# Kernel optimization log

Measured on AMD Instinct MI355X. Metric: run time of the kernel, lower is better.

Reference implementation:

```python
import jax, jax.numpy as jnp
from jax import lax
import numpy as np

B, S, T = 32, 512, 64
IN, H, L, HC, OUT = 512, 512, 2, 4, 512

def setup_inputs() -> dict:
    key = jax.random.key(0)
    ks = jax.random.split(key, 12)
    def w(k, shape, fan_in):
        return (jax.random.normal(k, shape, jnp.float32) / np.float32(np.sqrt(fan_in)))
    lstm_in0 = IN + HC * H
    return {
        "inputs": jax.random.normal(ks[0], (B, T, IN), jnp.float32),
        "lengths": jax.random.randint(ks[1], (B,), 1, S + 1),
        "final_hiddens": jax.random.normal(ks[2], (L, B, H), jnp.float32),
        "hiddens": jax.random.normal(ks[3], (B, S, H), jnp.float32),
        "max_output_len": T,
        "max_seq_len": S,
        "Wa1": w(ks[4], (H, 2 * H), 2 * H), "ba1": jnp.zeros((H,), jnp.float32),
        "Wa2": w(ks[5], (HC, H), H), "ba2": jnp.zeros((HC,), jnp.float32),
        "W_ih0": w(ks[6], (4 * H, lstm_in0), lstm_in0), "W_hh0": w(ks[7], (4 * H, H), H),
        "b_ih0": jnp.zeros((4 * H,), jnp.float32), "b_hh0": jnp.zeros((4 * H,), jnp.float32),
        "W_ih1": w(ks[8], (4 * H, H), H), "W_hh1": w(ks[9], (4 * H, H), H),
        "b_ih1": jnp.zeros((4 * H,), jnp.float32), "b_hh1": jnp.zeros((4 * H,), jnp.float32),
        "Wo1": w(ks[10], (H, (1 + HC) * H), (1 + HC) * H), "bo1": jnp.zeros((H,), jnp.float32),
        "Wo2": w(ks[11], (OUT, H), H), "bo2": jnp.zeros((OUT,), jnp.float32),
    }

def _lstm_cell(x, h, c, W_ih, W_hh, b_ih, b_hh):
    # PyTorch LSTM gate order: i, f, g, o
    g = x @ W_ih.T + b_ih + h @ W_hh.T + b_hh
    i, f, gg, o = jnp.split(g, 4, axis=-1)
    c_new = jax.nn.sigmoid(f) * c + jax.nn.sigmoid(i) * jnp.tanh(gg)
    h_new = jax.nn.sigmoid(o) * jnp.tanh(c_new)
    return h_new, c_new

def reference(inputs, lengths, final_hiddens, hiddens, max_output_len, max_seq_len,
              Wa1, ba1, Wa2, ba2, W_ih0, W_hh0, b_ih0, b_hh0,
              W_ih1, W_hh1, b_ih1, b_hh1, Wo1, bo1, Wo2, bo2):
    batch = inputs.shape[0]
    # r_mask[b, s] = 1 if s < lengths[b] else 0  -> [B, S, 1]
    r_mask = (jnp.arange(max_seq_len)[None, :] < lengths[:, None]).astype(hiddens.dtype)[..., None]

    def step(carry, x_t):
        h, c = carry  # each [L, B, H]
        last = h[-1]  # [B, H]
        dup = last[:, None, :] * r_mask  # [B, S, H]
        a = jax.nn.relu(jnp.concatenate([dup, hiddens], axis=2) @ Wa1.T + ba1)  # [B,S,H]
        a = jax.nn.relu(a @ Wa2.T + ba2)  # [B,S,HC]
        a = jax.nn.softmax(a, axis=1)  # softmax over seq dim (unmasked, as in source)
        c_vecs = jnp.einsum('bsk,bsh->bkh', a, hiddens).reshape(batch, -1)  # [B, HC*H]
        x = jnp.concatenate([x_t, c_vecs], axis=1)  # [B, IN + HC*H]
        h0, c0 = _lstm_cell(x, h[0], c[0], W_ih0, W_hh0, b_ih0, b_hh0)
        h1, c1 = _lstm_cell(h0, h[1], c[1], W_ih1, W_hh1, b_ih1, b_hh1)
        out = jnp.tanh(jax.nn.relu(jnp.concatenate([h1, c_vecs], axis=1) @ Wo1.T + bo1) @ Wo2.T + bo2)
        return (jnp.stack([h0, h1]), jnp.stack([c0, c1])), out

    c_init = jnp.zeros_like(final_hiddens)
    _, outs = lax.scan(step, (final_hiddens, c_init), jnp.swapaxes(inputs, 0, 1))  # [T,B,OUT]
    return jnp.swapaxes(outs, 0, 1)  # [B, T, OUT]
```

## Files before the change

### kernel.cpp

```cpp
#include <hip/hip_runtime.h>
#include <cmath>


typedef unsigned short ushort;
typedef unsigned int uint;
typedef __attribute__((ext_vector_type(8))) short bf16x8;
typedef __attribute__((ext_vector_type(4))) float f32x4;

__device__ __forceinline__ float sigmoidf_(float x) { return 1.f / (1.f + __expf(-x)); }
__device__ __forceinline__ float bf2f(ushort u) {
  union { uint i; float f; } x; x.i = ((uint)u) << 16; return x.f;
}
__device__ __forceinline__ ushort f2bf(float f) {
  union { float f; uint i; } x; x.f = f;
  return (ushort)((x.i + 0x7FFFu + ((x.i >> 16) & 1u)) >> 16);
}
__device__ __forceinline__ float wave_sum(float v) {
#pragma unroll
  for (int m = 1; m < 64; m <<= 1) v += __shfl_xor(v, m, 64);
  return v;
}
__device__ __forceinline__ float wave_max(float v) {
#pragma unroll
  for (int m = 1; m < 64; m <<= 1) v = fmaxf(v, __shfl_xor(v, m, 64));
  return v;
}

__global__ void __launch_bounds__(256) k_init(const float* __restrict__ fh,
                                              ushort* h0b0, ushort* h1b0,
                                              float* c0, float* c1) {
  int i = blockIdx.x * 256 + threadIdx.x;
  h0b0[i] = f2bf(fh[i]);
  h1b0[i] = f2bf(fh[16384 + i]);
  c0[i] = 0.f; c1[i] = 0.f;
}

__global__ void __launch_bounds__(256) k_prep(const float* __restrict__ hid,
                                              ushort* __restrict__ hbf) {
  size_t i0 = ((size_t)blockIdx.x * 256 + threadIdx.x) * 8;
  float4 f0 = *(const float4*)&hid[i0];
  float4 f1 = *(const float4*)&hid[i0 + 4];
  uint4 o;
  o.x = (uint)f2bf(f0.x) | ((uint)f2bf(f0.y) << 16);
  o.y = (uint)f2bf(f0.z) | ((uint)f2bf(f0.w) << 16);
  o.z = (uint)f2bf(f1.x) | ((uint)f2bf(f1.y) << 16);
  o.w = (uint)f2bf(f1.z) | ((uint)f2bf(f1.w) << 16);
  *(uint4*)&hbf[i0] = o;
}

__global__ void __launch_bounds__(256) k_inprep(const float* __restrict__ inputs,
                                                ushort* __restrict__ inb) {
  size_t idx4 = ((size_t)blockIdx.x * 256 + threadIdx.x) * 4;
  int m = (int)(idx4 >> 9), k = (int)(idx4 & 511);
  int b = m & 31, tt = m >> 5;
  float4 v = *(const float4*)&inputs[((size_t)b * 64 + tt) * 512 + k];
  ushort4 o; o.x = f2bf(v.x); o.y = f2bf(v.y); o.z = f2bf(v.z); o.w = f2bf(v.w);
  *(ushort4*)&inb[(size_t)m * 512 + k] = o;
}

__global__ void __launch_bounds__(256) k_wcvt(const float* __restrict__ W1, int ld1,
                                              const float* __restrict__ W2, int ld2,
                                              int split, int K,
                                              ushort* __restrict__ dst) {
  size_t idx = ((size_t)blockIdx.x * 256 + threadIdx.x) * 4;
  int j = (int)(idx / K), k = (int)(idx % K);
  const float* src = (k < split) ? (W1 + (size_t)j * ld1 + k)
                                 : (W2 + (size_t)j * ld2 + (k - split));
  float4 v = *(const float4*)src;
  ushort4 o; o.x = f2bf(v.x); o.y = f2bf(v.y); o.z = f2bf(v.z); o.w = f2bf(v.w);
  *(ushort4*)&dst[idx] = o;
}

__global__ void __launch_bounds__(256) k_hidproj(const float* __restrict__ hid,
                                                 const float* __restrict__ Wa1,
                                                 ushort* __restrict__ hpb) {
  __shared__ float As[64][33];
  __shared__ float Bs[64][33];
  int tid = threadIdx.x;
  int r0 = blockIdx.x * 64;
  int n0 = blockIdx.y * 64;
  int tm = (tid >> 4) << 2, tn = (tid & 15) << 2;
  int lr = tid >> 2, lk = (tid & 3) << 3;
  float acc[4][4] = {};
  for (int k0 = 0; k0 < 512; k0 += 32) {
    float4 a0 = *(const float4*)&hid[(size_t)(r0 + lr) * 512 + k0 + lk];
    float4 a1 = *(const float4*)&hid[(size_t)(r0 + lr) * 512 + k0 + lk + 4];
    float4 b0 = *(const float4*)&Wa1[(size_t)(n0 + lr) * 1024 + 512 + k0 + lk];
    float4 b1 = *(const float4*)&Wa1[(size_t)(n0 + lr) * 1024 + 512 + k0 + lk + 4];
    __syncthreads();
    As[lr][lk+0]=a0.x; As[lr][lk+1]=a0.y; As[lr][lk+2]=a0.z; As[lr][lk+3]=a0.w;
    As[lr][lk+4]=a1.x; As[lr][lk+5]=a1.y; As[lr][lk+6]=a1.z; As[lr][lk+7]=a1.w;
    Bs[lr][lk+0]=b0.x; Bs[lr][lk+1]=b0.y; Bs[lr][lk+2]=b0.z; Bs[lr][lk+3]=b0.w;
    Bs[lr][lk+4]=b1.x; Bs[lr][lk+5]=b1.y; Bs[lr][lk+6]=b1.z; Bs[lr][lk+7]=b1.w;
    __syncthreads();
#pragma unroll 8
    for (int kk = 0; kk < 32; kk++) {
      float av[4], bv[4];
#pragma unroll
      for (int i = 0; i < 4; i++) av[i] = As[tm + i][kk];
#pragma unroll
      for (int j = 0; j < 4; j++) bv[j] = Bs[tn + j][kk];
#pragma unroll
      for (int i = 0; i < 4; i++)
#pragma unroll
        for (int j = 0; j < 4; j++) acc[i][j] += av[i] * bv[j];
    }
  }
#pragma unroll
  for (int i = 0; i < 4; i++) {
    ushort4 o;
    o.x = f2bf(acc[i][0]); o.y = f2bf(acc[i][1]);
    o.z = f2bf(acc[i][2]); o.w = f2bf(acc[i][3]);
    *(ushort4*)&hpb[(size_t)(r0 + tm + i) * 512 + n0 + tn] = o;
  }
}

__device__ __forceinline__ void scores_accum(const ushort* __restrict__ hpr,
                                             const float* __restrict__ wa2s,
                                             const float* __restrict__ ba1s,
                                             const float* __restrict__ qs, float m,
                                             float& a0, float& a1, float& a2,
                                             float& a3) {
#pragma unroll
  for (int i8 = 0; i8 < 8; i8++) {
    bf16x8 hv8 = *(const bf16x8*)(hpr + i8 * 8);
#pragma unroll
    for (int e = 0; e < 8; e++) {
      int i = i8 * 8 + e;
      float a = fmaxf(bf2f(((ushort*)&hv8)[e]) + ba1s[i] + m * qs[i], 0.f);
      a0 += wa2s[i] * a;
      a1 += wa2s[64 + i] * a;
      a2 += wa2s[128 + i] * a;
      a3 += wa2s[192 + i] * a;
    }
  }
}

__global__ void __launch_bounds__(512) k_scst(const ushort* __restrict__ hpb,
                                              const float* __restrict__ ba1,
                                              const float* __restrict__ Wa2,
                                              float4* __restrict__ scoresP4) {
  __shared__ float wa2s[256], ba1s[64], qz[64];
  int bid = blockIdx.x, tid = threadIdx.x;
  int b = bid >> 3, kdq = bid & 7, kd0 = kdq << 6, s = tid;
  if (tid < 256) wa2s[tid] = Wa2[(tid >> 6) * 512 + kd0 + (tid & 63)];
  else if (tid < 320) ba1s[tid - 256] = ba1[kd0 + (tid - 256)];
  else if (tid < 384) qz[tid - 320] = 0.f;
  __syncthreads();
  float a0 = 0.f, a1 = 0.f, a2 = 0.f, a3 = 0.f;
  const ushort* hpr = hpb + (size_t)(b * 512 + s) * 512 + kd0;
  scores_accum(hpr, wa2s, ba1s, qz, 0.f, a0, a1, a2, a3);
  scoresP4[((size_t)(kdq * 32 + b)) * 512 + s] = make_float4(a0, a1, a2, a3);
}

__global__ void __launch_bounds__(512) k_sum0(const float4* __restrict__ scoresP4,
                                              const float* __restrict__ ba2,
                                              float* __restrict__ scores0) {
  int idx = blockIdx.x * 512 + threadIdx.x;
  int b = idx >> 9, s = idx & 511;
  float a0 = ba2[0], a1 = ba2[1], a2 = ba2[2], a3 = ba2[3];
#pragma unroll
  for (int q = 0; q < 8; q++) {
    float4 p = scoresP4[((size_t)(q * 32 + b)) * 512 + s];
    a0 += p.x; a1 += p.y; a2 += p.z; a3 += p.w;
  }
  scores0[((size_t)b * 4 + 0) * 512 + s] = fmaxf(a0, 0.f);
  scores0[((size_t)b * 4 + 1) * 512 + s] = fmaxf(a1, 0.f);
  scores0[((size_t)b * 4 + 2) * 512 + s] = fmaxf(a2, 0.f);
  scores0[((size_t)b * 4 + 3) * 512 + s] = fmaxf(a3, 0.f);
}

__global__ void __launch_bounds__(512) k_stat0(const float* __restrict__ scores0,
                                               const int* __restrict__ lengths,
                                               float* __restrict__ m0v,
                                               float* __restrict__ statZ,
                                               float* __restrict__ P0) {
  __shared__ float st[32], st2[32];
  int b = blockIdx.x, tid = threadIdx.x, lane = tid & 63, w = tid >> 6;
  int s = tid, len = lengths[b];
  bool stat = s >= len;
  float v[4], m0[4];
#pragma unroll
  for (int k = 0; k < 4; k++) v[k] = scores0[((size_t)b * 4 + k) * 512 + s];
#pragma unroll
  for (int k = 0; k < 4; k++) {
    float mk = wave_max(stat ? v[k] : -1e30f);
    if (lane == 0) st[w * 4 + k] = mk;
  }
  __syncthreads();
#pragma unroll
  for (int k = 0; k < 4; k++) {
    float m = st[k];
#pragma unroll
    for (int w2 = 1; w2 < 8; w2++) m = fmaxf(m, st[w2 * 4 + k]);
    m0[k] = m;
  }
  float e[4];
#pragma unroll
  for (int k = 0; k < 4; k++) {
    e[k] = stat ? __expf(v[k] - m0[k]) : 0.f;
    float sk = wave_sum(e[k]);
    if (lane == 0) st2[w * 4 + k] = sk;
  }
  __syncthreads();
#pragma unroll
  for (int k = 0; k < 4; k++) {
    P0[((size_t)b * 4 + k) * 512 + s] = e[k];
  }
  if (tid == 0) {
#pragma unroll
    for (int k = 0; k < 4; k++) {
      float z = 0.f;
#pragma unroll
      for (int w2 = 0; w2 < 8; w2++) z += st2[w2 * 4 + k];
      m0v[b * 4 + k] = m0[k];
      statZ[b * 4 + k] = z;
    }
  }
}

__global__ void __launch_bounds__(512) k_statvec(const float* __restrict__ P0,
                                                 const ushort* __restrict__ hbf,
                                                 const int* __restrict__ lengths,
                                                 float* __restrict__ statvec) {
  __shared__ float P[4 * 512];
  __shared__ float red2[8 * 256];
  int bid = blockIdx.x, tid = threadIdx.x;
  int b = bid >> 3, hs = bid & 7;
#pragma unroll
  for (int k = 0; k < 4; k++) P[k * 512 + tid] = P0[((size_t)b * 4 + k) * 512 + tid];
  __syncthreads();
  int h = tid & 63, w8 = tid >> 6;
  int len = lengths[b];
  float a0 = 0.f, a1 = 0.f, a2 = 0.f, a3 = 0.f;
  for (int si = len + ((w8 - len) & 7); si < 512; si += 8) {
    float hv = bf2f(hbf[((size_t)(b * 512 + si) * 512) + (hs << 6) + h]);
    a0 += P[si] * hv;
    a1 += P[512 + si] * hv;
    a2 += P[1024 + si] * hv;
    a3 += P[1536 + si] * hv;
  }
  red2[(w8 << 8) + h] = a0;
  red2[(w8 << 8) + 64 + h] = a1;
  red2[(w8 << 8) + 128 + h] = a2;
  red2[(w8 << 8) + 192 + h] = a3;
  __syncthreads();
  if (tid < 256) {
    int k = tid >> 6, hh = tid & 63;
    float acc = 0.f;
#pragma unroll
    for (int c = 0; c < 8; c++) acc += red2[(c << 8) + (k << 6) + hh];
    statvec[((size_t)b * 4 + k) * 512 + (hs << 6) + hh] = acc;
  }
}

__device__ __forceinline__ void mfma_slice(
    const ushort* __restrict__ W, int ldW, int jrow0, int jstride,
    const ushort* __restrict__ xA, int ldA, int xsplit,
    const ushort* __restrict__ xB, int ldB, int coff,
    int klo, int khi, float* __restrict__ redrow) {
  const int l = threadIdx.x & 63;
  const int r16 = l & 15, koff = (l >> 4) * 8;
  const int j = jrow0 + (r16 & 3) + (r16 >> 2) * jstride;
  const ushort* wrow = W + (size_t)j * ldW + koff;
  const ushort* a0A = xA + (size_t)r16 * ldA + koff;
  const ushort* a1A = xA + (size_t)(16 + r16) * ldA + koff;
  const ushort* a0B = xB + (size_t)r16 * ldB + koff;
  const ushort* a1B = xB + (size_t)(16 + r16) * ldB + koff;
  f32x4 acc0 = {0.f, 0.f, 0.f, 0.f}, acc1 = {0.f, 0.f, 0.f, 0.f};
#pragma unroll 4
  for (int k0 = klo; k0 < khi; k0 += 32) {
    bf16x8 av0, av1;
    if (k0 < xsplit) {
      av0 = *(const bf16x8*)(a0A + k0);
      av1 = *(const bf16x8*)(a1A + k0);
    } else {
      av0 = *(const bf16x8*)(a0B + (k0 - coff));
      av1 = *(const bf16x8*)(a1B + (k0 - coff));
    }
    bf16x8 wv = *(const bf16x8*)(wrow + k0);
    acc0 = __builtin_amdgcn_mfma_f32_16x16x32_bf16(av0, wv, acc0, 0, 0, 0);
    acc1 = __builtin_amdgcn_mfma_f32_16x16x32_bf16(av1, wv, acc1, 0, 0, 0);
  }
  const int brow = (l >> 4) << 2;
#pragma unroll
  for (int r = 0; r < 4; r++) {
    redrow[r16 * 33 + brow + r] = acc0[r];
    redrow[r16 * 33 + 16 + brow + r] = acc1[r];
  }
}

__global__ void __launch_bounds__(256) k_gin0(const ushort* __restrict__ Wg0b,
                                              const ushort* __restrict__ inb,
                                              float* __restrict__ gi0) {
  __shared__ float red[4 * 528];
  int tid = threadIdx.x, w = tid >> 6;
  int j0 = blockIdx.x * 16;
  for (int mt = 0; mt < 4; mt++) {
    int m0 = (blockIdx.y * 4 + mt) * 32;
    mfma_slice(Wg0b, 3072, j0, 4, inb + (size_t)m0 * 512, 512, 1 << 30,
               inb + (size_t)m0 * 512, 512, 0, w * 128, w * 128 + 128,
               red + w * 528);
    __syncthreads();
#pragma unroll
    for (int e = 0; e < 2; e++) {
      int idx = tid + e * 256;
      int j = idx >> 5, b = idx & 31;
      float v = 0.f;
#pragma unroll
      for (int ww = 0; ww < 4; ww++) v += red[ww * 528 + j * 33 + b];
      gi0[(size_t)(m0 + b) * 2048 + j0 + j] = v;
    }
    __syncthreads();
  }
}

__global__ void __launch_bounds__(512) k_scq(
    const ushort* __restrict__ Wq, const ushort* __restrict__ Wo1,
    const ushort* __restrict__ h1cur, const ushort* __restrict__ xb,
    const float* __restrict__ bo1, ushort* __restrict__ o1bf,
    const ushort* __restrict__ hpb, const float* __restrict__ ba1,
    const float* __restrict__ Wa2, const int* __restrict__ lengths,
    float4* __restrict__ scoresP4, int t) {
  __shared__ float red[8 * 528];
  __shared__ float qs[64], wa2s[256], ba1s[64];
  int bid = blockIdx.x, tid = threadIdx.x, w = tid >> 6, lane = tid & 63;
  if (bid < 32) {
    if (t < 1) return;
    mfma_slice(Wo1, 2560, bid * 16, 4, h1cur, 512, 512, xb, 2048, 512,
               w * 320, w * 320 + 320, red + w * 528);
    __syncthreads();
    int j = tid & 15, b = tid >> 4;
    float v = 0.f;
#pragma unroll
    for (int ww = 0; ww < 8; ww++) v += red[ww * 528 + j * 33 + b];
    int jj = bid * 16 + j;
    o1bf[b * 512 + jj] = f2bf(fmaxf(v + bo1[jj], 0.f));
  } else {
    if (t >= 64) return;
    int r = bid - 32;
    int b = r >> 3, kdq = r & 7, kd0 = kdq << 6;
    if (tid < 256) wa2s[tid] = Wa2[(tid >> 6) * 512 + kd0 + (tid & 63)];
    else if (tid < 320) ba1s[tid - 256] = ba1[kd0 + (tid - 256)];
    {
      bf16x8 hv8 = *(const bf16x8*)(h1cur + b * 512 + lane * 8);
      float hf[8];
#pragma unroll
      for (int e2 = 0; e2 < 8; e2++) hf[e2] = bf2f(((ushort*)&hv8)[e2]);
#pragma unroll
      for (int rr = 0; rr < 8; rr++) {
        int row = kd0 + w * 8 + rr;
        bf16x8 wv8 = *(const bf16x8*)(Wq + (size_t)row * 512 + lane * 8);
        float acc = 0.f;
#pragma unroll
        for (int e2 = 0; e2 < 8; e2++) acc += hf[e2] * bf2f(((ushort*)&wv8)[e2]);
        acc = wave_sum(acc);
        if (lane == 0) qs[w * 8 + rr] = acc;
      }
    }
    __syncthreads();
    int s = tid, len = lengths[b];
    if ((tid & ~63) >= len) return;
    float m = (s < len) ? 1.f : 0.f;
    float a0 = 0.f, a1 = 0.f, a2 = 0.f, a3 = 0.f;
    const ushort* hpr = hpb + (size_t)(b * 512 + s) * 512 + kd0;
    scores_accum(hpr, wa2s, ba1s, qs, m, a0, a1, a2, a3);
    scoresP4[((size_t)(kdq * 32 + b)) * 512 + s] = make_float4(a0, a1, a2, a3);
  }
}

__global__ void __launch_bounds__(512) k_ctxout(
    const float4* __restrict__ scoresP4, const float* __restrict__ ba2,
    const int* __restrict__ lengths, const ushort* __restrict__ hbf,
    const float* __restrict__ m0v, const float* __restrict__ statZ,
    const float* __restrict__ statvec, ushort* __restrict__ xb,
    const ushort* __restrict__ Wo2, const ushort* __restrict__ o1bf,
    const float* __restrict__ bo2, float* __restrict__ outp, int t) {
  __shared__ float red[8 * 528];
  __shared__ float P[4 * 512];
  __shared__ float red2[8 * 256];
  __shared__ float st[32], st2[32];
  int bid = blockIdx.x, tid = threadIdx.x;
  if (bid < 32) {
    if (t < 1) return;
    int w = tid >> 6;
    mfma_slice(Wo2, 512, bid * 16, 4, o1bf, 512, 1 << 30, o1bf, 512, 0,
               w * 64, w * 64 + 64, red + w * 528);
    __syncthreads();
    int j = tid & 15, b = tid >> 4;
    float v = 0.f;
#pragma unroll
    for (int ww = 0; ww < 8; ww++) v += red[ww * 528 + j * 33 + b];
    int jj = bid * 16 + j;
    outp[((size_t)b * 64 + (t - 1)) * 512 + jj] = tanhf(v + bo2[jj]);
  } else {
    if (t >= 64) return;
    int r = bid - 32;
    int b = r >> 3, hs = r & 7;
    int lane = tid & 63, w = tid >> 6;
    int s = tid, len = lengths[b];
    bool act = s < len;
    float v[4];
    {
      float a0 = ba2[0], a1 = ba2[1], a2 = ba2[2], a3 = ba2[3];
      if (act) {
#pragma unroll
        for (int q = 0; q < 8; q++) {
          float4 p = scoresP4[((size_t)(q * 32 + b)) * 512 + s];
          a0 += p.x; a1 += p.y; a2 += p.z; a3 += p.w;
        }
        v[0] = fmaxf(a0, 0.f); v[1] = fmaxf(a1, 0.f);
        v[2] = fmaxf(a2, 0.f); v[3] = fmaxf(a3, 0.f);
      } else {
        v[0] = v[1] = v[2] = v[3] = -1e30f;
      }
    }
    float M[4];
#pragma unroll
    for (int k = 0; k < 4; k++) {
      float mk = wave_max(v[k]);
      if (lane == 0) st[w * 4 + k] = mk;
    }
    __syncthreads();
#pragma unroll
    for (int k = 0; k < 4; k++) {
      float m = st[k];
#pragma unroll
      for (int w2 = 1; w2 < 8; w2++) m = fmaxf(m, st[w2 * 4 + k]);
      M[k] = fmaxf(m, m0v[b * 4 + k]);
    }
    float e[4];
#pragma unroll
    for (int k = 0; k < 4; k++) {
      e[k] = act ? __expf(v[k] - M[k]) : 0.f;
      float sk = wave_sum(e[k]);
      if (lane == 0) st2[w * 4 + k] = sk;
    }
    __syncthreads();
    float sc[4];
#pragma unroll
    for (int k = 0; k < 4; k++) {
      float dynZ = 0.f;
#pragma unroll
      for (int w2 = 0; w2 < 8; w2++) dynZ += st2[w2 * 4 + k];
      float scB = __expf(m0v[b * 4 + k] - M[k]);
      float Z = dynZ + scB * statZ[b * 4 + k];
      float invZ = 1.f / Z;
      P[k * 512 + s] = e[k] * invZ;
      sc[k] = scB * invZ;
    }
    __syncthreads();
    int h = tid & 63, w8 = tid >> 6;
    float a0 = 0.f, a1 = 0.f, a2 = 0.f, a3 = 0.f;
    const ushort* hb0 = hbf + ((size_t)b * 512) * 512 + (hs << 6) + h;
    int si = w8;
    for (; si + 24 < len; si += 32) {
      float h0v = bf2f(hb0[(size_t)si * 512]);
      float h1v = bf2f(hb0[(size_t)(si + 8) * 512]);
      float h2v = bf2f(hb0[(size_t)(si + 16) * 512]);
      float h3v = bf2f(hb0[(size_t)(si + 24) * 512]);
      a0 += P[si] * h0v + P[si + 8] * h1v + P[si + 16] * h2v + P[si + 24] * h3v;
      a1 += P[512 + si] * h0v + P[512 + si + 8] * h1v + P[512 + si + 16] * h2v +
            P[512 + si + 24] * h3v;
      a2 += P[1024 + si] * h0v + P[1024 + si + 8] * h1v + P[1024 + si + 16] * h2v +
            P[1024 + si + 24] * h3v;
      a3 += P[1536 + si] * h0v + P[1536 + si + 8] * h1v + P[1536 + si + 16] * h2v +
            P[1536 + si + 24] * h3v;
    }
    for (; si < len; si += 8) {
      float hv = bf2f(hb0[(size_t)si * 512]);
      a0 += P[si] * hv;
      a1 += P[512 + si] * hv;
      a2 += P[1024 + si] * hv;
      a3 += P[1536 + si] * hv;
    }
    red2[(w8 << 8) + h] = a0;
    red2[(w8 << 8) + 64 + h] = a1;
    red2[(w8 << 8) + 128 + h] = a2;
    red2[(w8 << 8) + 192 + h] = a3;
    __syncthreads();
    if (tid < 256) {
      int k = tid >> 6, hh = tid & 63;
      float acc = 0.f;
#pragma unroll
      for (int c = 0; c < 8; c++) acc += red2[(c << 8) + (k << 6) + hh];
      acc += sc[k] * statvec[((size_t)b * 4 + k) * 512 + (hs << 6) + hh];
      xb[b * 2048 + (k << 9) + (hs << 6) + hh] = f2bf(acc);
    }
  }
}

__global__ void __launch_bounds__(512) k_cell0(
    const ushort* __restrict__ Wg0b, const ushort* __restrict__ xb,
    const ushort* __restrict__ h0cur, const float* __restrict__ gi0,
    const float* __restrict__ bih, const float* __restrict__ bhh,
    float* __restrict__ cst, ushort* __restrict__ hnew, int t) {
  __shared__ float red[8 * 528];
  int bid = blockIdx.x, tid = threadIdx.x, w = tid >> 6;
  mfma_slice(Wg0b + 512, 3072, bid * 4, 512, xb, 2048, 2048, h0cur, 512, 2048,
             w * 320, w * 320 + 320, red + w * 528);
  __syncthreads();
  if (tid < 128) {
    int b = tid & 31, dh = tid >> 5;
    int h = bid * 4 + dh;
    float G[4];
#pragma unroll
    for (int g = 0; g < 4; g++) {
      float v = bih[g * 512 + h] + bhh[g * 512 + h] +
                gi0[(size_t)(t * 32 + b) * 2048 + g * 512 + h];
#pragma unroll
      for (int ww = 0; ww < 8; ww++) v += red[ww * 528 + (g * 4 + dh) * 33 + b];
      G[g] = v;
    }
    float i_ = sigmoidf_(G[0]), f_ = sigmoidf_(G[1]);
    float gg = tanhf(G[2]), o_ = sigmoidf_(G[3]);
    float cn = f_ * cst[b * 512 + h] + i_ * gg;
    cst[b * 512 + h] = cn;
    hnew[b * 512 + h] = f2bf(o_ * tanhf(cn));
  }
}

__global__ void __launch_bounds__(512) k_cell1(
    const ushort* __restrict__ Wg1b, const ushort* __restrict__ h0new,
    const ushort* __restrict__ h1cur, const float* __restrict__ bih,
    const float* __restrict__ bhh, float* __restrict__ cst,
    ushort* __restrict__ hnew) {
  __shared__ float red[8 * 528];
  int bid = blockIdx.x, tid = threadIdx.x, w = tid >> 6;
  mfma_slice(Wg1b, 1024, bid * 4, 512, h0new, 512, 512, h1cur, 512, 512,
             w * 128, w * 128 + 128, red + w * 528);
  __syncthreads();
  if (tid < 128) {
    int b = tid & 31, dh = tid >> 5;
    int h = bid * 4 + dh;
    float G[4];
#pragma unroll
    for (int g = 0; g < 4; g++) {
      float v = bih[g * 512 + h] + bhh[g * 512 + h];
#pragma unroll
      for (int ww = 0; ww < 8; ww++) v += red[ww * 528 + (g * 4 + dh) * 33 + b];
      G[g] = v;
    }
    float i_ = sigmoidf_(G[0]), f_ = sigmoidf_(G[1]);
    float gg = tanhf(G[2]), o_ = sigmoidf_(G[3]);
    float cn = f_ * cst[b * 512 + h] + i_ * gg;
    cst[b * 512 + h] = cn;
    hnew[b * 512 + h] = f2bf(o_ * tanhf(cn));
  }
}

extern "C" void kernel_launch(void* const* d_in, const int* in_sizes, int n_in,
                              void* d_out, int out_size, void* d_ws, size_t ws_size,
                              hipStream_t stream) {
  const float* inputs  = (const float*)d_in[0];
  const int*   lengths = (const int*)d_in[1];
  const float* fh      = (const float*)d_in[2];
  const float* hiddens = (const float*)d_in[3];
  const float* Wa1  = (const float*)d_in[6];
  const float* ba1  = (const float*)d_in[7];
  const float* Wa2  = (const float*)d_in[8];
  const float* ba2  = (const float*)d_in[9];
  const float* Wih0 = (const float*)d_in[10];
  const float* Whh0 = (const float*)d_in[11];
  const float* bih0 = (const float*)d_in[12];
  const float* bhh0 = (const float*)d_in[13];
  const float* Wih1 = (const float*)d_in[14];
  const float* Whh1 = (const float*)d_in[15];
  const float* bih1 = (const float*)d_in[16];
  const float* bhh1 = (const float*)d_in[17];
  const float* Wo1  = (const float*)d_in[18];
  const float* bo1  = (const float*)d_in[19];
  const float* Wo2  = (const float*)d_in[20];
  const float* bo2  = (const float*)d_in[21];
  float* outp = (float*)d_out;

  char* p = (char*)d_ws;
  ushort* hpb = (ushort*)p; p += (size_t)32 * 512 * 512 * 2;
  ushort* hbf = (ushort*)p; p += (size_t)32 * 512 * 512 * 2;
  float4* scoresP4 = (float4*)p; p += (size_t)8 * 32 * 512 * 16;
  float* scores0 = (float*)p; p += (size_t)32 * 4 * 512 * 4;
  float* P0      = (float*)p; p += (size_t)32 * 4 * 512 * 4;
  float* statvec = (float*)p; p += (size_t)32 * 4 * 512 * 4;
  float* m0v     = (float*)p; p += 128 * sizeof(float);
  float* statZ   = (float*)p; p += 128 * sizeof(float);
  ushort* xb     = (ushort*)p; p += (size_t)32 * 2048 * 2;
  ushort* h0b    = (ushort*)p; p += (size_t)2 * 32 * 512 * 2;
  ushort* h1b    = (ushort*)p; p += (size_t)2 * 32 * 512 * 2;
  ushort* o1bf   = (ushort*)p; p += (size_t)32 * 512 * 2;
  float* c0      = (float*)p; p += (size_t)32 * 512 * 4;
  float* c1      = (float*)p; p += (size_t)32 * 512 * 4;
  ushort* Wg0b   = (ushort*)p; p += (size_t)2048 * 3072 * 2;
  ushort* Wg1b   = (ushort*)p; p += (size_t)2048 * 1024 * 2;
  ushort* Wo1b   = (ushort*)p; p += (size_t)512 * 2560 * 2;
  ushort* Wo2b   = (ushort*)p; p += (size_t)512 * 512 * 2;
  ushort* Wqb    = (ushort*)p; p += (size_t)512 * 512 * 2;
  ushort* inb    = (ushort*)p; p += (size_t)2048 * 512 * 2;
  float* gi0     = (float*)p; p += (size_t)2048 * 2048 * 4;

  k_init<<<64, 256, 0, stream>>>(fh, h0b, h1b, c0, c1);
  k_prep<<<4096, 256, 0, stream>>>(hiddens, hbf);
  k_inprep<<<1024, 256, 0, stream>>>(inputs, inb);
  k_hidproj<<<dim3(256, 8), 256, 0, stream>>>(hiddens, Wa1, hpb);
  k_wcvt<<<6144, 256, 0, stream>>>(Wih0, 2560, Whh0, 512, 2560, 3072, Wg0b);
  k_wcvt<<<2048, 256, 0, stream>>>(Wih1, 512, Whh1, 512, 512, 1024, Wg1b);
  k_wcvt<<<1280, 256, 0, stream>>>(Wo1, 2560, Wo1, 2560, 2560, 2560, Wo1b);
  k_wcvt<<<256, 256, 0, stream>>>(Wo2, 512, Wo2, 512, 512, 512, Wo2b);
  k_wcvt<<<256, 256, 0, stream>>>(Wa1, 1024, Wa1, 1024, 512, 512, Wqb);
  k_gin0<<<dim3(128, 16), 256, 0, stream>>>(Wg0b, inb, gi0);
  k_scst<<<256, 512, 0, stream>>>(hpb, ba1, Wa2, scoresP4);
  k_sum0<<<32, 512, 0, stream>>>(scoresP4, ba2, scores0);
  k_stat0<<<32, 512, 0, stream>>>(scores0, lengths, m0v, statZ, P0);
  k_statvec<<<256, 512, 0, stream>>>(P0, hbf, lengths, statvec);

  for (int t = 0; t <= 64; t++) {
    const ushort* h1cur = h1b + (size_t)(t & 1) * 16384;
    const ushort* h0cur = h0b + (size_t)(t & 1) * 16384;
    ushort* h0nxt = h0b + (size_t)((t + 1) & 1) * 16384;
    ushort* h1nxt = h1b + (size_t)((t + 1) & 1) * 16384;
    k_scq<<<288, 512, 0, stream>>>(Wqb, Wo1b, h1cur, xb, bo1, o1bf, hpb, ba1,
                                   Wa2, lengths, scoresP4, t);
    k_ctxout<<<288, 512, 0, stream>>>(scoresP4, ba2, lengths, hbf, m0v, statZ,
                                      statvec, xb, Wo2b, o1bf, bo2, outp, t);
    if (t < 64) {
      k_cell0<<<128, 512, 0, stream>>>(Wg0b, xb, h0cur, gi0, bih0, bhh0, c0,
                                       h0nxt, t);
      k_cell1<<<128, 512, 0, stream>>>(Wg1b, h0nxt, h1cur, bih1, bhh1, c1, h1nxt);
    }
  }
}
```

Measured before the change: 2.987 ms.

## Fuse attention scoring, softmax and context into one per-batch kernel; merge Wo2 into cell0

Replaces the separate score kernel (k_scq) and context kernel (k_ctxout) with a single k_attn kernel. It uses one 1024-thread block per batch row that computes the query projection, the scores, the masked softmax and the context vector entirely in shared memory, so the scoresP4 round trip through global memory goes away. The Wo2 output projection moves into the cell0 launch as extra blocks, and xb becomes double-buffered so the Wo1 projection from the previous step can run alongside. This cuts per-step launches from four to three and removes global traffic. In exchange, attention parallelism drops from 256 blocks to 32 blocks of 1024 threads, and those blocks use a large amount of shared memory.

```diff
diff --git a/kernel.cpp b/kernel.cpp
--- a/kernel.cpp
+++ b/kernel.cpp
@@ -115,41 +115,31 @@
   }
 }
 
-__device__ __forceinline__ void scores_accum(const ushort* __restrict__ hpr,
-                                             const float* __restrict__ wa2s,
-                                             const float* __restrict__ ba1s,
-                                             const float* __restrict__ qs, float m,
-                                             float& a0, float& a1, float& a2,
-                                             float& a3) {
+__global__ void __launch_bounds__(512) k_scst(const ushort* __restrict__ hpb,
+                                              const float* __restrict__ ba1,
+                                              const float* __restrict__ Wa2,
+                                              float4* __restrict__ scoresP4) {
+  __shared__ float wa2s[256], ba1s[64];
+  int bid = blockIdx.x, tid = threadIdx.x;
+  int b = bid >> 3, kdq = bid & 7, kd0 = kdq << 6, s = tid;
+  if (tid < 256) wa2s[tid] = Wa2[(tid >> 6) * 512 + kd0 + (tid & 63)];
+  else if (tid < 320) ba1s[tid - 256] = ba1[kd0 + (tid - 256)];
+  __syncthreads();
+  float a0 = 0.f, a1 = 0.f, a2 = 0.f, a3 = 0.f;
+  const ushort* hpr = hpb + (size_t)(b * 512 + s) * 512 + kd0;
 #pragma unroll
   for (int i8 = 0; i8 < 8; i8++) {
     bf16x8 hv8 = *(const bf16x8*)(hpr + i8 * 8);
 #pragma unroll
     for (int e = 0; e < 8; e++) {
       int i = i8 * 8 + e;
-      float a = fmaxf(bf2f(((ushort*)&hv8)[e]) + ba1s[i] + m * qs[i], 0.f);
+      float a = fmaxf(bf2f(((ushort*)&hv8)[e]) + ba1s[i], 0.f);
       a0 += wa2s[i] * a;
       a1 += wa2s[64 + i] * a;
       a2 += wa2s[128 + i] * a;
       a3 += wa2s[192 + i] * a;
     }
   }
-}
-
-__global__ void __launch_bounds__(512) k_scst(const ushort* __restrict__ hpb,
-                                              const float* __restrict__ ba1,
-                                              const float* __restrict__ Wa2,
-                                              float4* __restrict__ scoresP4) {
-  __shared__ float wa2s[256], ba1s[64], qz[64];
-  int bid = blockIdx.x, tid = threadIdx.x;
-  int b = bid >> 3, kdq = bid & 7, kd0 = kdq << 6, s = tid;
-  if (tid < 256) wa2s[tid] = Wa2[(tid >> 6) * 512 + kd0 + (tid & 63)];
-  else if (tid < 320) ba1s[tid - 256] = ba1[kd0 + (tid - 256)];
-  else if (tid < 384) qz[tid - 320] = 0.f;
-  __syncthreads();
-  float a0 = 0.f, a1 = 0.f, a2 = 0.f, a3 = 0.f;
-  const ushort* hpr = hpb + (size_t)(b * 512 + s) * 512 + kd0;
-  scores_accum(hpr, wa2s, ba1s, qz, 0.f, a0, a1, a2, a3);
   scoresP4[((size_t)(kdq * 32 + b)) * 512 + s] = make_float4(a0, a1, a2, a3);
 }
 
@@ -315,129 +305,111 @@
   }
 }
 
-__global__ void __launch_bounds__(512) k_scq(
-    const ushort* __restrict__ Wq, const ushort* __restrict__ Wo1,
-    const ushort* __restrict__ h1cur, const ushort* __restrict__ xb,
-    const float* __restrict__ bo1, ushort* __restrict__ o1bf,
-    const ushort* __restrict__ hpb, const float* __restrict__ ba1,
-    const float* __restrict__ Wa2, const int* __restrict__ lengths,
-    float4* __restrict__ scoresP4, int t) {
+__global__ void __launch_bounds__(1024) k_attn(
+    const ushort* __restrict__ Wq, const ushort* __restrict__ hpb,
+    const float* __restrict__ ba1, const float* __restrict__ Wa2,
+    const float* __restrict__ ba2, const int* __restrict__ lengths,
+    const float* __restrict__ m0v, const float* __restrict__ statZ,
+    const float* __restrict__ statvec, const ushort* __restrict__ hbf,
+    const ushort* __restrict__ h1cur, ushort* __restrict__ xbcur,
+    const ushort* __restrict__ Wo1, const ushort* __restrict__ xbprev,
+    const float* __restrict__ bo1, ushort* __restrict__ o1bf, int t) {
   __shared__ float red[8 * 528];
-  __shared__ float qs[64], wa2s[256], ba1s[64];
-  int bid = blockIdx.x, tid = threadIdx.x, w = tid >> 6, lane = tid & 63;
-  if (bid < 32) {
-    if (t < 1) return;
-    mfma_slice(Wo1, 2560, bid * 16, 4, h1cur, 512, 512, xb, 2048, 512,
-               w * 320, w * 320 + 320, red + w * 528);
+  __shared__ float wa2s[2048], ba1s[512], qpart[1024], qs[512];
+  __shared__ float scpart[4096], P[2048], red2[4096];
+  __shared__ float st[32], st2[32], sc_l[4];
+  int bid = blockIdx.x, tid = threadIdx.x;
+  if (bid >= 32) {
+    bool act = (t >= 1) && (tid < 512);
+    int w = tid >> 6;
+    if (act)
+      mfma_slice(Wo1, 2560, (bid - 32) * 16, 4, h1cur, 512, 512, xbprev, 2048,
+                 512, w * 320, w * 320 + 320, red + w * 528);
     __syncthreads();
-    int j = tid & 15, b = tid >> 4;
-    float v = 0.f;
-#pragma unroll
-    for (int ww = 0; ww < 8; ww++) v += red[ww * 528 + j * 33 + b];
-    int jj = bid * 16 + j;
-    o1bf[b * 512 + jj] = f2bf(fmaxf(v + bo1[jj], 0.f));
-  } else {
-    if (t >= 64) return;
-    int r = bid - 32;
-    int b = r >> 3, kdq = r & 7, kd0 = kdq << 6;
-    if (tid < 256) wa2s[tid] = Wa2[(tid >> 6) * 512 + kd0 + (tid & 63)];
-    else if (tid < 320) ba1s[tid - 256] = ba1[kd0 + (tid - 256)];
-    {
-      bf16x8 hv8 = *(const bf16x8*)(h1cur + b * 512 + lane * 8);
-      float hf[8];
-#pragma unroll
-      for (int e2 = 0; e2 < 8; e2++) hf[e2] = bf2f(((ushort*)&hv8)[e2]);
-#pragma unroll
-      for (int rr = 0; rr < 8; rr++) {
-        int row = kd0 + w * 8 + rr;
-        bf16x8 wv8 = *(const bf16x8*)(Wq + (size_t)row * 512 + lane * 8);
-        float acc = 0.f;
-#pragma unroll
-        for (int e2 = 0; e2 < 8; e2++) acc += hf[e2] * bf2f(((ushort*)&wv8)[e2]);
-        acc = wave_sum(acc);
-        if (lane == 0) qs[w * 8 + rr] = acc;
+    if (act && tid < 512) {
+      int j = tid & 15, b = tid >> 4;
+      float v = 0.f;
+#pragma unroll
+      for (int ww = 0; ww < 8; ww++) v += red[ww * 528 + j * 33 + b];
+      int jj = (bid - 32) * 16 + j;
+      o1bf[b * 512 + jj] = f2bf(fmaxf(v + bo1[jj], 0.f));
+    }
+    return;
+  }
+  if (t >= 64) return;
+  const int b = bid;
+  const int rw = tid & 511, half = tid >> 9;
+  const int lane = tid & 63, w = tid >> 6;
+  const int len = lengths[b];
+  for (int i = tid; i < 2048; i += 1024) wa2s[i] = Wa2[(i >> 9) * 512 + (i & 511)];
+  if (tid < 512) ba1s[tid] = ba1[tid];
+  {
+    const ushort* h1r = h1cur + b * 512 + half * 256;
+    const ushort* wr = Wq + (size_t)rw * 512 + half * 256;
+    float acc = 0.f;
+#pragma unroll
+    for (int i = 0; i < 32; i++) {
+      bf16x8 wv = *(const bf16x8*)(wr + i * 8);
+      bf16x8 hv = *(const bf16x8*)(h1r + i * 8);
+#pragma unroll
+      for (int e = 0; e < 8; e++)
+        acc += bf2f(((ushort*)&hv)[e]) * bf2f(((ushort*)&wv)[e]);
+    }
+    qpart[half * 512 + rw] = acc;
+  }
+  __syncthreads();
+  if (tid < 512) qs[tid] = qpart[tid] + qpart[512 + tid];
+  __syncthreads();
+  {
+    float a0 = 0.f, a1 = 0.f, a2 = 0.f, a3 = 0.f;
+    if (rw < len) {
+      const ushort* hpr = hpb + (size_t)(b * 512 + rw) * 512 + half * 256;
+      const int kb = half * 256;
+#pragma unroll
+      for (int i8 = 0; i8 < 32; i8++) {
+        bf16x8 hv8 = *(const bf16x8*)(hpr + i8 * 8);
+#pragma unroll
+        for (int e = 0; e < 8; e++) {
+          int i = kb + i8 * 8 + e;
+          float a = fmaxf(bf2f(((ushort*)&hv8)[e]) + ba1s[i] + qs[i], 0.f);
+          a0 += wa2s[i] * a;
+          a1 += wa2s[512 + i] * a;
+          a2 += wa2s[1024 + i] * a;
+          a3 += wa2s[1536 + i] * a;
+        }
       }
     }
-    __syncthreads();
-    int s = tid, len = lengths[b];
-    if ((tid & ~63) >= len) return;
-    float m = (s < len) ? 1.f : 0.f;
-    float a0 = 0.f, a1 = 0.f, a2 = 0.f, a3 = 0.f;
-    const ushort* hpr = hpb + (size_t)(b * 512 + s) * 512 + kd0;
-    scores_accum(hpr, wa2s, ba1s, qs, m, a0, a1, a2, a3);
-    scoresP4[((size_t)(kdq * 32 + b)) * 512 + s] = make_float4(a0, a1, a2, a3);
-  }
-}
-
-__global__ void __launch_bounds__(512) k_ctxout(
-    const float4* __restrict__ scoresP4, const float* __restrict__ ba2,
-    const int* __restrict__ lengths, const ushort* __restrict__ hbf,
-    const float* __restrict__ m0v, const float* __restrict__ statZ,
-    const float* __restrict__ statvec, ushort* __restrict__ xb,
-    const ushort* __restrict__ Wo2, const ushort* __restrict__ o1bf,
-    const float* __restrict__ bo2, float* __restrict__ outp, int t) {
-  __shared__ float red[8 * 528];
-  __shared__ float P[4 * 512];
-  __shared__ float red2[8 * 256];
-  __shared__ float st[32], st2[32];
-  int bid = blockIdx.x, tid = threadIdx.x;
-  if (bid < 32) {
-    if (t < 1) return;
-    int w = tid >> 6;
-    mfma_slice(Wo2, 512, bid * 16, 4, o1bf, 512, 1 << 30, o1bf, 512, 0,
-               w * 64, w * 64 + 64, red + w * 528);
-    __syncthreads();
-    int j = tid & 15, b = tid >> 4;
-    float v = 0.f;
-#pragma unroll
-    for (int ww = 0; ww < 8; ww++) v += red[ww * 528 + j * 33 + b];
-    int jj = bid * 16 + j;
-    outp[((size_t)b * 64 + (t - 1)) * 512 + jj] = tanhf(v + bo2[jj]);
-  } else {
-    if (t >= 64) return;
-    int r = bid - 32;
-    int b = r >> 3, hs = r & 7;
-    int lane = tid & 63, w = tid >> 6;
-    int s = tid, len = lengths[b];
-    bool act = s < len;
-    float v[4];
-    {
-      float a0 = ba2[0], a1 = ba2[1], a2 = ba2[2], a3 = ba2[3];
-      if (act) {
-#pragma unroll
-        for (int q = 0; q < 8; q++) {
-          float4 p = scoresP4[((size_t)(q * 32 + b)) * 512 + s];
-          a0 += p.x; a1 += p.y; a2 += p.z; a3 += p.w;
-        }
-        v[0] = fmaxf(a0, 0.f); v[1] = fmaxf(a1, 0.f);
-        v[2] = fmaxf(a2, 0.f); v[3] = fmaxf(a3, 0.f);
-      } else {
-        v[0] = v[1] = v[2] = v[3] = -1e30f;
-      }
-    }
-    float M[4];
+    float* sp = scpart + half * 2048;
+    sp[rw] = a0; sp[512 + rw] = a1; sp[1024 + rw] = a2; sp[1536 + rw] = a3;
+  }
+  __syncthreads();
+  float v[4], M[4], e[4];
+  bool act = rw < len;
+  if (tid < 512) {
 #pragma unroll
     for (int k = 0; k < 4; k++) {
+      v[k] = act ? fmaxf(scpart[k * 512 + rw] + scpart[2048 + k * 512 + rw] +
+                             ba2[k], 0.f)
+                 : -1e30f;
       float mk = wave_max(v[k]);
       if (lane == 0) st[w * 4 + k] = mk;
     }
-    __syncthreads();
+  }
+  __syncthreads();
+  if (tid < 512) {
 #pragma unroll
     for (int k = 0; k < 4; k++) {
       float m = st[k];
 #pragma unroll
       for (int w2 = 1; w2 < 8; w2++) m = fmaxf(m, st[w2 * 4 + k]);
       M[k] = fmaxf(m, m0v[b * 4 + k]);
-    }
-    float e[4];
-#pragma unroll
-    for (int k = 0; k < 4; k++) {
       e[k] = act ? __expf(v[k] - M[k]) : 0.f;
       float sk = wave_sum(e[k]);
       if (lane == 0) st2[w * 4 + k] = sk;
     }
-    __syncthreads();
-    float sc[4];
+  }
+  __syncthreads();
+  if (tid < 512) {
 #pragma unroll
     for (int k = 0; k < 4; k++) {
       float dynZ = 0.f;
@@ -446,77 +418,94 @@
       float scB = __expf(m0v[b * 4 + k] - M[k]);
       float Z = dynZ + scB * statZ[b * 4 + k];
       float invZ = 1.f / Z;
-      P[k * 512 + s] = e[k] * invZ;
-      sc[k] = scB * invZ;
-    }
-    __syncthreads();
-    int h = tid & 63, w8 = tid >> 6;
+      P[k * 512 + rw] = e[k] * invZ;
+      if (tid == 0) sc_l[k] = scB * invZ;
+    }
+  }
+  __syncthreads();
+  {
     float a0 = 0.f, a1 = 0.f, a2 = 0.f, a3 = 0.f;
-    const ushort* hb0 = hbf + ((size_t)b * 512) * 512 + (hs << 6) + h;
-    int si = w8;
-    for (; si + 24 < len; si += 32) {
+    const ushort* hb0 = hbf + ((size_t)b * 512) * 512 + rw;
+    int si = half;
+    for (; si + 6 < len; si += 8) {
       float h0v = bf2f(hb0[(size_t)si * 512]);
-      float h1v = bf2f(hb0[(size_t)(si + 8) * 512]);
-      float h2v = bf2f(hb0[(size_t)(si + 16) * 512]);
-      float h3v = bf2f(hb0[(size_t)(si + 24) * 512]);
-      a0 += P[si] * h0v + P[si + 8] * h1v + P[si + 16] * h2v + P[si + 24] * h3v;
-      a1 += P[512 + si] * h0v + P[512 + si + 8] * h1v + P[512 + si + 16] * h2v +
-            P[512 + si + 24] * h3v;
-      a2 += P[1024 + si] * h0v + P[1024 + si + 8] * h1v + P[1024 + si + 16] * h2v +
-            P[1024 + si + 24] * h3v;
-      a3 += P[1536 + si] * h0v + P[1536 + si + 8] * h1v + P[1536 + si + 16] * h2v +
-            P[1536 + si + 24] * h3v;
-    }
-    for (; si < len; si += 8) {
+      float h1v = bf2f(hb0[(size_t)(si + 2) * 512]);
+      float h2v = bf2f(hb0[(size_t)(si + 4) * 512]);
+      float h3v = bf2f(hb0[(size_t)(si + 6) * 512]);
+      a0 += P[si] * h0v + P[si + 2] * h1v + P[si + 4] * h2v + P[si + 6] * h3v;
+      a1 += P[512 + si] * h0v + P[514 + si] * h1v + P[516 + si] * h2v +
+            P[518 + si] * h3v;
+      a2 += P[1024 + si] * h0v + P[1026 + si] * h1v + P[1028 + si] * h2v +
+            P[1030 + si] * h3v;
+      a3 += P[1536 + si] * h0v + P[1538 + si] * h1v + P[1540 + si] * h2v +
+            P[1542 + si] * h3v;
+    }
+    for (; si < len; si += 2) {
       float hv = bf2f(hb0[(size_t)si * 512]);
       a0 += P[si] * hv;
       a1 += P[512 + si] * hv;
       a2 += P[1024 + si] * hv;
       a3 += P[1536 + si] * hv;
     }
-    red2[(w8 << 8) + h] = a0;
-    red2[(w8 << 8) + 64 + h] = a1;
-    red2[(w8 << 8) + 128 + h] = a2;
-    red2[(w8 << 8) + 192 + h] = a3;
-    __syncthreads();
-    if (tid < 256) {
-      int k = tid >> 6, hh = tid & 63;
-      float acc = 0.f;
-#pragma unroll
-      for (int c = 0; c < 8; c++) acc += red2[(c << 8) + (k << 6) + hh];
-      acc += sc[k] * statvec[((size_t)b * 4 + k) * 512 + (hs << 6) + hh];
-      xb[b * 2048 + (k << 9) + (hs << 6) + hh] = f2bf(acc);
-    }
-  }
-}
-
-__global__ void __launch_bounds__(512) k_cell0(
-    const ushort* __restrict__ Wg0b, const ushort* __restrict__ xb,
+    float* r2 = red2 + half * 2048;
+    r2[rw] = a0; r2[512 + rw] = a1; r2[1024 + rw] = a2; r2[1536 + rw] = a3;
+  }
+  __syncthreads();
+  {
+#pragma unroll
+    for (int e2 = 0; e2 < 2; e2++) {
+      int k = half * 2 + e2;
+      float acc = red2[k * 512 + rw] + red2[2048 + k * 512 + rw] +
+                  sc_l[k] * statvec[((size_t)b * 4 + k) * 512 + rw];
+      xbcur[b * 2048 + k * 512 + rw] = f2bf(acc);
+    }
+  }
+}
+
+__global__ void __launch_bounds__(512) k_cell0out(
+    const ushort* __restrict__ Wg0b, const ushort* __restrict__ xbcur,
     const ushort* __restrict__ h0cur, const float* __restrict__ gi0,
     const float* __restrict__ bih, const float* __restrict__ bhh,
-    float* __restrict__ cst, ushort* __restrict__ hnew, int t) {
+    float* __restrict__ cst, ushort* __restrict__ hnew,
+    const ushort* __restrict__ Wo2, const ushort* __restrict__ o1bf,
+    const float* __restrict__ bo2, float* __restrict__ outp, int t) {
   __shared__ float red[8 * 528];
   int bid = blockIdx.x, tid = threadIdx.x, w = tid >> 6;
-  mfma_slice(Wg0b + 512, 3072, bid * 4, 512, xb, 2048, 2048, h0cur, 512, 2048,
-             w * 320, w * 320 + 320, red + w * 528);
-  __syncthreads();
-  if (tid < 128) {
-    int b = tid & 31, dh = tid >> 5;
-    int h = bid * 4 + dh;
-    float G[4];
-#pragma unroll
-    for (int g = 0; g < 4; g++) {
-      float v = bih[g * 512 + h] + bhh[g * 512 + h] +
-                gi0[(size_t)(t * 32 + b) * 2048 + g * 512 + h];
-#pragma unroll
-      for (int ww = 0; ww < 8; ww++) v += red[ww * 528 + (g * 4 + dh) * 33 + b];
-      G[g] = v;
-    }
-    float i_ = sigmoidf_(G[0]), f_ = sigmoidf_(G[1]);
-    float gg = tanhf(G[2]), o_ = sigmoidf_(G[3]);
-    float cn = f_ * cst[b * 512 + h] + i_ * gg;
-    cst[b * 512 + h] = cn;
-    hnew[b * 512 + h] = f2bf(o_ * tanhf(cn));
+  if (bid < 128) {
+    if (t >= 64) return;
+    mfma_slice(Wg0b + 512, 3072, bid * 4, 512, xbcur, 2048, 2048, h0cur, 512,
+               2048, w * 320, w * 320 + 320, red + w * 528);
+    __syncthreads();
+    if (tid < 128) {
+      int b = tid & 31, dh = tid >> 5;
+      int h = bid * 4 + dh;
+      float G[4];
+#pragma unroll
+      for (int g = 0; g < 4; g++) {
+        float v = bih[g * 512 + h] + bhh[g * 512 + h] +
+                  gi0[(size_t)(t * 32 + b) * 2048 + g * 512 + h];
+#pragma unroll
+        for (int ww = 0; ww < 8; ww++) v += red[ww * 528 + (g * 4 + dh) * 33 + b];
+        G[g] = v;
+      }
+      float i_ = sigmoidf_(G[0]), f_ = sigmoidf_(G[1]);
+      float gg = tanhf(G[2]), o_ = sigmoidf_(G[3]);
+      float cn = f_ * cst[b * 512 + h] + i_ * gg;
+      cst[b * 512 + h] = cn;
+      hnew[b * 512 + h] = f2bf(o_ * tanhf(cn));
+    }
+  } else {
+    if (t < 1) return;
+    int jm = bid - 128;
+    mfma_slice(Wo2, 512, jm * 16, 4, o1bf, 512, 1 << 30, o1bf, 512, 0,
+               w * 64, w * 64 + 64, red + w * 528);
+    __syncthreads();
+    int j = tid & 15, b = tid >> 4;
+    float v = 0.f;
+#pragma unroll
+    for (int ww = 0; ww < 8; ww++) v += red[ww * 528 + j * 33 + b];
+    int jj = jm * 16 + j;
+    outp[((size_t)b * 64 + (t - 1)) * 512 + jj] = tanhf(v + bo2[jj]);
   }
 }
 
@@ -583,7 +572,7 @@
   float* statvec = (float*)p; p += (size_t)32 * 4 * 512 * 4;
   float* m0v     = (float*)p; p += 128 * sizeof(float);
   float* statZ   = (float*)p; p += 128 * sizeof(float);
-  ushort* xb     = (ushort*)p; p += (size_t)32 * 2048 * 2;
+  ushort* xbuf   = (ushort*)p; p += (size_t)2 * 32 * 2048 * 2;
   ushort* h0b    = (ushort*)p; p += (size_t)2 * 32 * 512 * 2;
   ushort* h1b    = (ushort*)p; p += (size_t)2 * 32 * 512 * 2;
   ushort* o1bf   = (ushort*)p; p += (size_t)32 * 512 * 2;
@@ -617,14 +606,16 @@
     const ushort* h0cur = h0b + (size_t)(t & 1) * 16384;
     ushort* h0nxt = h0b + (size_t)((t + 1) & 1) * 16384;
     ushort* h1nxt = h1b + (size_t)((t + 1) & 1) * 16384;
-    k_scq<<<288, 512, 0, stream>>>(Wqb, Wo1b, h1cur, xb, bo1, o1bf, hpb, ba1,
-                                   Wa2, lengths, scoresP4, t);
-    k_ctxout<<<288, 512, 0, stream>>>(scoresP4, ba2, lengths, hbf, m0v, statZ,
-                                      statvec, xb, Wo2b, o1bf, bo2, outp, t);
+    ushort* xbcur = xbuf + (size_t)(t & 1) * 65536;
+    ushort* xbprev = xbuf + (size_t)((t + 1) & 1) * 65536;
+    k_attn<<<64, 1024, 0, stream>>>(Wqb, hpb, ba1, Wa2, ba2, lengths, m0v,
+                                    statZ, statvec, hbf, h1cur, xbcur, Wo1b,
+                                    xbprev, bo1, o1bf, t);
+    k_cell0out<<<160, 512, 0, stream>>>(Wg0b, xbcur, h0cur, gi0, bih0, bhh0,
+                                        c0, h0nxt, Wo2b, o1bf, bo2, outp, t);
     if (t < 64) {
-      k_cell0<<<128, 512, 0, stream>>>(Wg0b, xb, h0cur, gi0, bih0, bhh0, c0,
-                                       h0nxt, t);
-      k_cell1<<<128, 512, 0, stream>>>(Wg1b, h0nxt, h1cur, bih1, bhh1, c1, h1nxt);
-    }
-  }
-}
+      k_cell1<<<128, 512, 0, stream>>>(Wg1b, h0nxt, h1cur, bih1, bhh1, c1,
+                                       h1nxt);
+    }
+  }
+}
```

Result: slower. 5.660 ms (+89.5%).
